# Kernel tuning notes

Hardware: AMD Instinct MI355X
Metric: run time of the kernel (lower is better)

## Reference

```python
import jax, jax.numpy as jnp
import numpy as np

N = 50000
E = 1600000
IN_C = 32
OUT_C = 32
OUT_SIZE = 1


def setup_inputs() -> dict:
    key = jax.random.key(0)
    ks = jax.random.split(key, 16)
    x = jax.random.normal(ks[0], (N, IN_C), dtype=jnp.float32)
    edge_index = jax.random.randint(ks[1], (2, E), 0, N, dtype=jnp.int64)

    def glorot(k, shape):
        lim = float(np.sqrt(6.0 / (shape[0] + shape[1])))
        return jax.random.uniform(k, shape, jnp.float32, -lim, lim)

    params = {
        # GCNConv weights for gates z, r, h: [in, out] and bias [out]
        'Wz_c': glorot(ks[2], (IN_C, OUT_C)), 'bz_c': jnp.zeros((OUT_C,), jnp.float32),
        'Wr_c': glorot(ks[3], (IN_C, OUT_C)), 'br_c': jnp.zeros((OUT_C,), jnp.float32),
        'Wh_c': glorot(ks[4], (IN_C, OUT_C)), 'bh_c': jnp.zeros((OUT_C,), jnp.float32),
        # GRU linear layers: [2*out, out] and bias [out]
        'Wz_l': glorot(ks[5], (2 * OUT_C, OUT_C)), 'bz_l': jnp.zeros((OUT_C,), jnp.float32),
        'Wr_l': glorot(ks[6], (2 * OUT_C, OUT_C)), 'br_l': jnp.zeros((OUT_C,), jnp.float32),
        'Wh_l': glorot(ks[7], (2 * OUT_C, OUT_C)), 'bh_l': jnp.zeros((OUT_C,), jnp.float32),
        # final readout Linear(out_channels, output_size)
        'W_lin': glorot(ks[8], (OUT_C, OUT_SIZE)), 'b_lin': jnp.zeros((OUT_SIZE,), jnp.float32),
    }
    return {'x': x, 'edge_index': edge_index, **params}


def _gcn_conv(x, W, b, src, dst, n_nodes):
    """GCNConv with add_self_loops=False, symmetric normalization."""
    h = x @ W  # [N, out]
    ones = jnp.ones((src.shape[0],), h.dtype)
    deg = jax.ops.segment_sum(ones, dst, num_segments=n_nodes)  # in-degree at targets
    dinv = jnp.where(deg > 0, jax.lax.rsqrt(jnp.maximum(deg, 1e-12)), 0.0)
    norm = dinv[src] * dinv[dst]  # [E]
    msg = h[src] * norm[:, None]  # gather + scale
    agg = jax.ops.segment_sum(msg, dst, num_segments=n_nodes)  # scatter-add
    return agg + b


def reference(x, edge_index, Wz_c, bz_c, Wr_c, br_c, Wh_c, bh_c,
              Wz_l, bz_l, Wr_l, br_l, Wh_l, bh_l, W_lin, b_lin):
    src, dst = edge_index[0], edge_index[1]
    n = x.shape[0]
    H = jnp.zeros((n, OUT_C), x.dtype)  # H=None -> zeros

    Z = jax.nn.sigmoid(jnp.concatenate([_gcn_conv(x, Wz_c, bz_c, src, dst, n), H], axis=1) @ Wz_l + bz_l)
    R = jax.nn.sigmoid(jnp.concatenate([_gcn_conv(x, Wr_c, br_c, src, dst, n), H], axis=1) @ Wr_l + br_l)
    H_tilde = jnp.tanh(jnp.concatenate([_gcn_conv(x, Wh_c, bh_c, src, dst, n), H * R], axis=1) @ Wh_l + bh_l)
    H = Z * H + (1.0 - Z) * H_tilde

    h = jax.nn.relu(H)
    return h @ W_lin + b_lin  # [N, output_size]
```

## Files before the change

### kernel.cpp

```cpp
#include <hip/hip_runtime.h>
#include <hip/hip_fp16.h>
#include <math.h>

#define NN 50000
#define NE 1600000
#define ELLW 80
#define SHN 6250
#define XH_WORDS 800000

#define NBIN 400
#define BINW 125
#define NSUB 8
#define SUBCAP 680
#define MAGIC125 34359739u

#define OFF_ELL 0
#define NEED_A ((4000000ull + 800000 + 800000 + 50000 + 2112) * 4)
#define NEED_B ((4000000ull + 800000 + 50000 + 2112) * 4)

struct h2x2 { __half2 a, b; };

__global__ __launch_bounds__(1024) void init_kernel(
        const float* __restrict__ Wz_c, const float* __restrict__ bz_c,
        const float* __restrict__ Wh_c, const float* __restrict__ bh_c,
        const float* __restrict__ Wz_l, const float* __restrict__ bz_l,
        const float* __restrict__ Wh_l, const float* __restrict__ bh_l,
        float* __restrict__ Mz, float* __restrict__ Mh,
        float* __restrict__ cz, float* __restrict__ ch,
        unsigned int* __restrict__ bcur,
        const float* __restrict__ x, __half2* __restrict__ xh) {
    int t = threadIdx.x;
    if (blockIdx.x == 0) {
        int i = t >> 5, j = t & 31;
        float az = 0.0f, ah = 0.0f;
        for (int k = 0; k < 32; ++k) {
            az += Wz_c[i * 32 + k] * Wz_l[k * 32 + j];
            ah += Wh_c[i * 32 + k] * Wh_l[k * 32 + j];
        }
        Mz[i * 32 + j] = az;
        Mh[i * 32 + j] = ah;
        if (i == 0) {
            float sz = bz_l[j], sh = bh_l[j];
            for (int k = 0; k < 32; ++k) {
                sz += bz_c[k] * Wz_l[k * 32 + j];
                sh += bh_c[k] * Wh_l[k * 32 + j];
            }
            cz[j] = sz;
            ch[j] = sh;
        }
        return;
    }
    if (blockIdx.x == 1) {
        for (int i = t; i < NBIN * NSUB; i += 1024) bcur[i] = 0u;
    }
    if (xh) {
        int idx = (blockIdx.x - 1) * 1024 + t;
        int stride = (gridDim.x - 1) * 1024;
        const float2* x2 = (const float2*)x;
        for (int i = idx; i < XH_WORDS; i += stride) {
            float2 v = x2[i];
            xh[i] = __floats2half2_rn(v.x, v.y);
        }
    }
}

__global__ __launch_bounds__(512) void bucket_kernel(const int* __restrict__ ei,
                                                     unsigned int* __restrict__ bcur,
                                                     unsigned int* __restrict__ bkt) {
    __shared__ unsigned int lcnt[NBIN];
    __shared__ unsigned int lstart[NBIN];
    __shared__ unsigned int loff[NBIN];
    __shared__ unsigned int gbase[NBIN];
    __shared__ unsigned int stage[2048];
    int t = threadIdx.x;
    for (int i = t; i < NBIN; i += 512) lcnt[i] = 0u;
    __syncthreads();
    int i4 = blockIdx.x * 512 + t;
    bool valid = (i4 < NE / 4);
    int4 s4 = make_int4(0, 0, 0, 0), d4 = make_int4(0, 0, 0, 0);
    if (valid) {
        s4 = ((const int4*)ei)[i4];
        d4 = ((const int4*)(ei + NE))[i4];
#define CNT_E(dd)                                                           \
        if ((unsigned)(dd) < NN)                                            \
            atomicAdd(&lcnt[__umulhi((unsigned)(dd), MAGIC125)], 1u);
        CNT_E(d4.x) CNT_E(d4.y) CNT_E(d4.z) CNT_E(d4.w)
#undef CNT_E
    }
    __syncthreads();
    if (t < NBIN) loff[t] = lcnt[t];
    __syncthreads();
    for (int off = 1; off < NBIN; off <<= 1) {
        unsigned v = 0;
        if (t < NBIN && t >= off) v = loff[t - off];
        __syncthreads();
        if (t < NBIN) loff[t] += v;
        __syncthreads();
    }
    int g = blockIdx.x & (NSUB - 1);
    if (t < NBIN) {
        lstart[t] = loff[t] - lcnt[t];
        gbase[t] = lcnt[t] ? atomicAdd(&bcur[t * NSUB + g], lcnt[t]) : 0u;
    }
    __syncthreads();
    if (t < NBIN) loff[t] = lstart[t];
    __syncthreads();
    if (valid) {
#define SC_E(dd, ss)                                                        \
        if ((unsigned)(dd) < NN && (unsigned)(ss) < NN) {                   \
            unsigned bn = __umulhi((unsigned)(dd), MAGIC125);               \
            unsigned p = atomicAdd(&loff[bn], 1u);                          \
            stage[p] = ((unsigned)(dd) << 16) | (unsigned)(ss);             \
        }
        SC_E(d4.x, s4.x) SC_E(d4.y, s4.y) SC_E(d4.z, s4.z) SC_E(d4.w, s4.w)
#undef SC_E
    }
    __syncthreads();
    unsigned tot = loff[NBIN - 1];
    for (unsigned i = t; i < tot; i += 512) {
        unsigned v = stage[i];
        unsigned bn = __umulhi(v >> 16, MAGIC125);
        unsigned gg = gbase[bn] + (i - lstart[bn]);
        if (gg < SUBCAP) bkt[(bn * NSUB + g) * SUBCAP + gg] = v;
    }
}

__global__ __launch_bounds__(256) void build_ell_kernel(const unsigned int* __restrict__ bkt,
                                                        const unsigned int* __restrict__ bcur,
                                                        unsigned int* __restrict__ cnt,
                                                        float* __restrict__ dinv,
                                                        unsigned short* __restrict__ ell) {
    __shared__ unsigned int lcnt[BINW];
    __shared__ alignas(16) unsigned short stage[BINW * ELLW];
    int t = threadIdx.x;
    int b = blockIdx.x;
    int bin = (b & 7) * 50 + (b >> 3);
    int nbase = bin * BINW;
    for (int i = t; i < BINW; i += 256) lcnt[i] = 0u;
    __syncthreads();
    for (int g = 0; g < NSUB; ++g) {
        unsigned tot = bcur[bin * NSUB + g];
        if (tot > SUBCAP) tot = SUBCAP;
        const unsigned int* bp = bkt + (bin * NSUB + g) * SUBCAP;
        for (unsigned i = t; i < tot; i += 256) {
            unsigned v = bp[i];
            unsigned ld = (v >> 16) - (unsigned)nbase;
            unsigned p = atomicAdd(&lcnt[ld], 1u);
            if (p < ELLW) stage[ld * ELLW + p] = (unsigned short)(v & 0xffffu);
        }
    }
    __syncthreads();
    const uint2* st2 = (const uint2*)stage;
    uint2* ell2 = (uint2*)(ell + (size_t)nbase * ELLW);
    for (int i = t; i < BINW * ELLW / 4; i += 256) ell2[i] = st2[i];
    for (int i = t; i < BINW; i += 256) {
        unsigned d = lcnt[i];
        cnt[nbase + i] = d;
        dinv[nbase + i] = d ? rsqrtf((float)d) : 0.0f;
    }
}

template <int USE_H>
__global__ __launch_bounds__(256) void gather_node_kernel(const unsigned short* __restrict__ ell,
                                                          const unsigned int* __restrict__ cnt,
                                                          const float* __restrict__ dinv,
                                                          const float* __restrict__ x,
                                                          const h2x2* __restrict__ xh,
                                                          const float* __restrict__ Mz,
                                                          const float* __restrict__ Mh,
                                                          const float* __restrict__ cz,
                                                          const float* __restrict__ ch,
                                                          const float* __restrict__ Wlin,
                                                          const float* __restrict__ blin,
                                                          float* __restrict__ out) {
    __shared__ float sMz[1024], sMh[1024], scz[32], sch[32], sw[32];
    __shared__ float xs[4][32];
    int t = threadIdx.x;
    for (int i = t; i < 1024; i += 256) { sMz[i] = Mz[i]; sMh[i] = Mh[i]; }
    if (t < 32) { scz[t] = cz[t]; sch[t] = ch[t]; sw[t] = Wlin[t]; }
    __syncthreads();

    int w  = t >> 6;
    int l  = t & 63;
    int shard = blockIdx.x & 7;
    int grp   = blockIdx.x >> 3;
    int ns = grp * 4 + w;
    if (ns >= SHN) return;
    int n = shard * SHN + ns;

    int base = n * ELLW;
    int len0 = (int)cnt[n];
    float dn = len0 ? rsqrtf((float)len0) : 0.0f;
    int len = len0 > ELLW ? ELLW : len0;

    const float4* x4 = (const float4*)x;
    int es = l >> 3;
    int k  = l & 7;
    float4 acc = make_float4(0.f, 0.f, 0.f, 0.f);

    for (int c0 = 0; c0 < len; c0 += 64) {
        int m = len - c0; if (m > 64) m = 64;
        int s = 0; float wgt = 0.0f;
        if (l < m) { s = (int)ell[base + c0 + l]; wgt = dinv[s]; }
#define SW(j0) { int je = (j0) + es; int sj = __shfl(s, je); float wj = __shfl(wgt, je);   \
                 if (USE_H) {                                                              \
                     h2x2 hv = xh[sj * 8 + k];                                             \
                     float2 f0 = __half22float2(hv.a), f1 = __half22float2(hv.b);          \
                     acc.x += f0.x * wj; acc.y += f0.y * wj;                               \
                     acc.z += f1.x * wj; acc.w += f1.y * wj;                               \
                 } else {                                                                  \
                     float4 v = x4[sj * 8 + k];                                            \
                     acc.x += v.x * wj; acc.y += v.y * wj;                                 \
                     acc.z += v.z * wj; acc.w += v.w * wj;                                 \
                 } }
        SW(0) SW(8)
        if (m > 16) { SW(16) SW(24) }
        if (m > 32) { SW(32) SW(40) }
        if (m > 48) { SW(48) SW(56) }
#undef SW
    }
    #pragma unroll
    for (int mm = 8; mm < 64; mm <<= 1) {
        acc.x += __shfl_xor(acc.x, mm);
        acc.y += __shfl_xor(acc.y, mm);
        acc.z += __shfl_xor(acc.z, mm);
        acc.w += __shfl_xor(acc.w, mm);
    }
    if (es == 0) {
        float4* xs4 = (float4*)&xs[w][0];
        xs4[k] = make_float4(acc.x * dn, acc.y * dn, acc.z * dn, acc.w * dn);
    }

    int j = l & 31, half = l >> 5;
    float az = half ? 0.0f : scz[j];
    float ah = half ? 0.0f : sch[j];
    int ibase = half * 16;
    #pragma unroll
    for (int ii = 0; ii < 16; ++ii) {
        int i = ibase + ii;
        float v = xs[w][i];
        az += v * sMz[i * 32 + j];
        ah += v * sMh[i * 32 + j];
    }
    az += __shfl_xor(az, 32);
    ah += __shfl_xor(ah, 32);
    float z  = 1.0f / (1.0f + __expf(-az));
    float ht = tanhf(ah);
    float hv = (1.0f - z) * ht;
    hv = hv > 0.0f ? hv : 0.0f;
    float val = hv * sw[j];
    val += __shfl_xor(val, 1, 32);
    val += __shfl_xor(val, 2, 32);
    val += __shfl_xor(val, 4, 32);
    val += __shfl_xor(val, 8, 32);
    val += __shfl_xor(val, 16, 32);
    if (l == 0) out[n] = val + blin[0];
}

extern "C" void kernel_launch(void* const* d_in, const int* in_sizes, int n_in,
                              void* d_out, int out_size, void* d_ws, size_t ws_size,
                              hipStream_t stream) {
    const float* x    = (const float*)d_in[0];
    const int*   ei   = (const int*)d_in[1];
    const float* Wz_c = (const float*)d_in[2];
    const float* bz_c = (const float*)d_in[3];
    const float* Wh_c = (const float*)d_in[6];
    const float* bh_c = (const float*)d_in[7];
    const float* Wz_l = (const float*)d_in[8];
    const float* bz_l = (const float*)d_in[9];
    const float* Wh_l = (const float*)d_in[12];
    const float* bh_l = (const float*)d_in[13];
    const float* Wlin = (const float*)d_in[14];
    const float* blin = (const float*)d_in[15];
    float* out = (float*)d_out;
    float* ws = (float*)d_ws;

    int use_h = (ws_size >= NEED_A) ? 1 : 0;

    unsigned short* ell16 = (unsigned short*)(ws + OFF_ELL);
    unsigned int*   cnt   = (unsigned int*)(ws + 2000000);
    __half2*        xh    = use_h ? (__half2*)(ws + 2050000) : nullptr;
    float*          dinv  = ws + 2050000 + (use_h ? XH_WORDS : 0);
    float*          Mz    = dinv + NN;
    float*          Mh    = Mz + 1024;
    float*          cz    = Mh + 1024;
    float*          ch    = cz + 32;
    unsigned int*   bkt   = (unsigned int*)(ch + 32);
    unsigned int*   bcur  = bkt + (size_t)NBIN * NSUB * SUBCAP;

    const int bucket_grid = (NE / 4 + 511) / 512;
    const int build_grid  = NBIN;
    const int node_grid   = 8 * ((SHN + 3) / 4);
    const int init_grid   = 1 + 256;

    init_kernel<<<init_grid, 1024, 0, stream>>>(Wz_c, bz_c, Wh_c, bh_c,
                                                Wz_l, bz_l, Wh_l, bh_l,
                                                Mz, Mh, cz, ch, bcur, x, xh);
    bucket_kernel<<<bucket_grid, 512, 0, stream>>>(ei, bcur, bkt);
    build_ell_kernel<<<build_grid, 256, 0, stream>>>(bkt, bcur, cnt, dinv, ell16);
    if (use_h) {
        gather_node_kernel<1><<<node_grid, 256, 0, stream>>>(
            ell16, cnt, dinv, x, (const h2x2*)xh, Mz, Mh, cz, ch, Wlin, blin, out);
    } else {
        gather_node_kernel<0><<<node_grid, 256, 0, stream>>>(
            ell16, cnt, dinv, x, (const h2x2*)nullptr, Mz, Mh, cz, ch, Wlin, blin, out);
    }
}
```

Before: 160.1 us.

## Map two nodes per wavefront with half-wave gather and matvec

Each 64-lane wavefront now handles two destination nodes, one per 32-lane half, instead of one node per wave. The neighbor loop walks chunks of 32 edges with 4 edges per step and runs to the longer of the two halves' lengths. The dense GRU matvec is done by a single half-wave over all 32 inputs, which removes the cross-half reduction. With about 50 neighbors on average, this is meant to cut idle lanes and halve the block count, at the cost of divergence when the two nodes' degrees differ and a longer serial matvec per lane.

```diff
diff --git a/kernel.cpp b/kernel.cpp
--- a/kernel.cpp
+++ b/kernel.cpp
@@ -174,17 +174,19 @@
                                                           const float* __restrict__ blin,
                                                           float* __restrict__ out) {
     __shared__ float sMz[1024], sMh[1024], scz[32], sch[32], sw[32];
-    __shared__ float xs[4][32];
+    __shared__ float xs[8][32];
     int t = threadIdx.x;
     for (int i = t; i < 1024; i += 256) { sMz[i] = Mz[i]; sMh[i] = Mh[i]; }
     if (t < 32) { scz[t] = cz[t]; sch[t] = ch[t]; sw[t] = Wlin[t]; }
     __syncthreads();
 
-    int w  = t >> 6;
-    int l  = t & 63;
+    int l    = t & 63;
+    int slot = t >> 5;
+    int q    = l & 31;
+    int hb   = l & 32;
     int shard = blockIdx.x & 7;
     int grp   = blockIdx.x >> 3;
-    int ns = grp * 4 + w;
+    int ns = grp * 8 + slot;
     if (ns >= SHN) return;
     int n = shard * SHN + ns;
 
@@ -192,17 +194,19 @@
     int len0 = (int)cnt[n];
     float dn = len0 ? rsqrtf((float)len0) : 0.0f;
     int len = len0 > ELLW ? ELLW : len0;
+    int lenW = max(len, __shfl_xor(len, 32));
 
     const float4* x4 = (const float4*)x;
-    int es = l >> 3;
-    int k  = l & 7;
+    int es = q >> 3;
+    int k  = q & 7;
     float4 acc = make_float4(0.f, 0.f, 0.f, 0.f);
 
-    for (int c0 = 0; c0 < len; c0 += 64) {
-        int m = len - c0; if (m > 64) m = 64;
+    for (int c0 = 0; c0 < lenW; c0 += 32) {
+        int m = len - c0; if (m > 32) m = 32;
+        int mw = lenW - c0; if (mw > 32) mw = 32;
         int s = 0; float wgt = 0.0f;
-        if (l < m) { s = (int)ell[base + c0 + l]; wgt = dinv[s]; }
-#define SW(j0) { int je = (j0) + es; int sj = __shfl(s, je); float wj = __shfl(wgt, je);   \
+        if (q < m) { s = (int)ell[base + c0 + q]; wgt = dinv[s]; }
+#define SW(j0) { int sl = hb + (j0) + es; int sj = __shfl(s, sl); float wj = __shfl(wgt, sl); \
                  if (USE_H) {                                                              \
                      h2x2 hv = xh[sj * 8 + k];                                             \
                      float2 f0 = __half22float2(hv.a), f1 = __half22float2(hv.b);          \
@@ -213,48 +217,44 @@
                      acc.x += v.x * wj; acc.y += v.y * wj;                                 \
                      acc.z += v.z * wj; acc.w += v.w * wj;                                 \
                  } }
-        SW(0) SW(8)
-        if (m > 16) { SW(16) SW(24) }
-        if (m > 32) { SW(32) SW(40) }
-        if (m > 48) { SW(48) SW(56) }
+        SW(0) SW(4)
+        if (mw > 8)  { SW(8)  SW(12) }
+        if (mw > 16) { SW(16) SW(20) }
+        if (mw > 24) { SW(24) SW(28) }
 #undef SW
     }
     #pragma unroll
-    for (int mm = 8; mm < 64; mm <<= 1) {
+    for (int mm = 8; mm <= 16; mm <<= 1) {
         acc.x += __shfl_xor(acc.x, mm);
         acc.y += __shfl_xor(acc.y, mm);
         acc.z += __shfl_xor(acc.z, mm);
         acc.w += __shfl_xor(acc.w, mm);
     }
     if (es == 0) {
-        float4* xs4 = (float4*)&xs[w][0];
+        float4* xs4 = (float4*)&xs[slot][0];
         xs4[k] = make_float4(acc.x * dn, acc.y * dn, acc.z * dn, acc.w * dn);
     }
 
-    int j = l & 31, half = l >> 5;
-    float az = half ? 0.0f : scz[j];
-    float ah = half ? 0.0f : sch[j];
-    int ibase = half * 16;
+    int j = q;
+    float az = scz[j];
+    float ah = sch[j];
     #pragma unroll
-    for (int ii = 0; ii < 16; ++ii) {
-        int i = ibase + ii;
-        float v = xs[w][i];
+    for (int i = 0; i < 32; ++i) {
+        float v = xs[slot][i];
         az += v * sMz[i * 32 + j];
         ah += v * sMh[i * 32 + j];
     }
-    az += __shfl_xor(az, 32);
-    ah += __shfl_xor(ah, 32);
     float z  = 1.0f / (1.0f + __expf(-az));
     float ht = tanhf(ah);
     float hv = (1.0f - z) * ht;
     hv = hv > 0.0f ? hv : 0.0f;
     float val = hv * sw[j];
-    val += __shfl_xor(val, 1, 32);
-    val += __shfl_xor(val, 2, 32);
-    val += __shfl_xor(val, 4, 32);
-    val += __shfl_xor(val, 8, 32);
-    val += __shfl_xor(val, 16, 32);
-    if (l == 0) out[n] = val + blin[0];
+    val += __shfl_xor(val, 1);
+    val += __shfl_xor(val, 2);
+    val += __shfl_xor(val, 4);
+    val += __shfl_xor(val, 8);
+    val += __shfl_xor(val, 16);
+    if (q == 0) out[n] = val + blin[0];
 }
 
 extern "C" void kernel_launch(void* const* d_in, const int* in_sizes, int n_in,
@@ -290,7 +290,7 @@
 
     const int bucket_grid = (NE / 4 + 511) / 512;
     const int build_grid  = NBIN;
-    const int node_grid   = 8 * ((SHN + 3) / 4);
+    const int node_grid   = 8 * ((SHN + 7) / 8);
     const int init_grid   = 1 + 256;
 
     init_kernel<<<init_grid, 1024, 0, stream>>>(Wz_c, bz_c, Wh_c, bh_c,
```

New measurement: 159.5 us. About the same (-0.4%).
